# Kernel optimization log

Measured on AMD Instinct MI355X. Metric: run time of the kernel, lower is better.

Reference implementation:

```python
import jax, jax.numpy as jnp
import numpy as np

B = 2048
D = 256
TEMPERATURE = 0.5
EPS = 1e-8  # torch.nn.CosineSimilarity eps


def _neg_indices(b):
    # Static mask: exclude diagonal and positive pairs (i, B+i), (B+i, i).
    n = 2 * b
    mask = np.ones((n, n), dtype=bool)
    np.fill_diagonal(mask, False)
    idx = np.arange(b)
    mask[idx, b + idx] = False
    mask[b + idx, idx] = False
    rows, cols = np.nonzero(mask)  # row-major order, matches torch sim[mask]
    return rows.reshape(n, n - 2), cols.reshape(n, n - 2)

_NEG_ROWS, _NEG_COLS = _neg_indices(B)


def setup_inputs() -> dict:
    key = jax.random.key(0)
    k1, k2 = jax.random.split(key)
    z_i = jax.random.normal(k1, (B, D), dtype=jnp.float32)
    z_j = jax.random.normal(k2, (B, D), dtype=jnp.float32)
    return {"z_i": z_i, "z_j": z_j}


def reference(z_i, z_j):
    b = z_i.shape[0]
    n = 2 * b
    z = jnp.concatenate([z_i, z_j], axis=0)  # [N, D]
    # Cosine similarity = normalize -> matmul (same math as broadcast CosineSimilarity)
    norm = jnp.maximum(jnp.linalg.norm(z, axis=1, keepdims=True), EPS)
    zn = z / norm
    sim = (zn @ zn.T) / TEMPERATURE  # [N, N]
    # positives: diag(sim, B) and diag(sim, -B)
    pos = jnp.concatenate([jnp.diagonal(sim, offset=b), jnp.diagonal(sim, offset=-b)], axis=0)  # [N]
    # negatives: static masked gather -> [N, N-2]
    neg = sim[_NEG_ROWS, _NEG_COLS]
    logits = jnp.concatenate([pos[:, None], neg], axis=1)  # [N, N-1]
    # CrossEntropyLoss(reduction='sum') with labels all zero, then / N
    loss = -jax.nn.log_softmax(logits, axis=1)[:, 0]
    return jnp.sum(loss) / n
```

## Files before the change

### kernel.cpp

```cpp
#include <hip/hip_runtime.h>
#include <hip/hip_bf16.h>
#include <math.h>

#define B_PAIRS 2048
#define N_ROWS  4096
#define D_DIM   256
#define INV_T   2.0f

typedef __attribute__((ext_vector_type(8))) short  short8;
typedef __attribute__((ext_vector_type(4))) float  floatx4;


__device__ __forceinline__ void async_copy16(const void* gsrc, void* ldst) {
    __builtin_amdgcn_global_load_lds(
        (__attribute__((address_space(1))) void*)gsrc,
        (__attribute__((address_space(3))) void*)ldst,
        16, 0, 0);
}

__global__ __launch_bounds__(256)
void ntx_normalize(const float* __restrict__ z_i,
                   const float* __restrict__ z_j,
                   __hip_bfloat16* __restrict__ zn,
                   float* __restrict__ S) {
    const int w    = threadIdx.x >> 6;
    const int lane = threadIdx.x & 63;
    const int row  = blockIdx.x * 4 + w;
    const float* src = (row < B_PAIRS) ? (z_i + (size_t)row * D_DIM)
                                       : (z_j + (size_t)(row - B_PAIRS) * D_DIM);
    const float4 v = *(const float4*)(src + lane * 4);
    float ss = v.x * v.x + v.y * v.y + v.z * v.z + v.w * v.w;
    #pragma unroll
    for (int off = 32; off > 0; off >>= 1) ss += __shfl_xor(ss, off, 64);
    const float rn = 1.0f / fmaxf(sqrtf(ss), 1e-8f);
    union { short4 s4; __hip_bfloat16 h[4]; } u;
    u.h[0] = __float2bfloat16(v.x * rn);
    u.h[1] = __float2bfloat16(v.y * rn);
    u.h[2] = __float2bfloat16(v.z * rn);
    u.h[3] = __float2bfloat16(v.w * rn);
    *(short4*)(void*)(zn + (size_t)row * D_DIM + lane * 4) = u.s4;
    if (lane == 0) S[row] = 0.0f;
}

#define BM 128
#define BN 128
#define BK 32
#define N_TILES 528

__global__ __launch_bounds__(256)
void ntx_simtile(const __hip_bfloat16* __restrict__ zn,
                 float* __restrict__ S,
                 float* __restrict__ pos) {
    __shared__ __align__(16) __hip_bfloat16 As[BM * BK];
    __shared__ __align__(16) __hip_bfloat16 Bs[BN * BK];

    int t = blockIdx.x, by = 0, rowlen = 32;
    while (t >= rowlen) { t -= rowlen; by++; rowlen--; }
    const int bx = by + t;

    const int tid  = threadIdx.x;
    const int lane = tid & 63;
    const int w    = tid >> 6;
    const int wr   = w >> 1;
    const int wc   = w & 1;
    const int quad = lane >> 4;
    const int l16  = lane & 15;

    const int rowA0 = by * BM;
    const int rowB0 = bx * BN;
    const bool isDiag = (rowA0 == rowB0);
    const bool isPos  = (rowB0 == (rowA0 ^ B_PAIRS));

    floatx4 acc[4][4];
    #pragma unroll
    for (int i = 0; i < 4; i++)
        #pragma unroll
        for (int j = 0; j < 4; j++)
            acc[i][j] = (floatx4){0.f, 0.f, 0.f, 0.f};

    for (int k0 = 0; k0 < D_DIM; k0 += BK) {
        #pragma unroll
        for (int c = 0; c < 2; c++) {
            const int chunk = tid + c * 256;
            const int r  = chunk >> 2;
            const int kc = chunk & 3;
            async_copy16(zn + ((size_t)(rowA0 + r) * D_DIM + k0 + kc * 8),
                         As + chunk * 8);
            async_copy16(zn + ((size_t)(rowB0 + r) * D_DIM + k0 + kc * 8),
                         Bs + chunk * 8);
        }
        __syncthreads();

        short8 afr[4], bfr[4];
        #pragma unroll
        for (int fi = 0; fi < 4; fi++) {
            const int ar = wr * 64 + fi * 16 + l16;
            afr[fi] = *(const short8*)(const void*)(As + ar * BK + quad * 8);
        }
        #pragma unroll
        for (int fj = 0; fj < 4; fj++) {
            const int brw = wc * 64 + fj * 16 + l16;
            bfr[fj] = *(const short8*)(const void*)(Bs + brw * BK + quad * 8);
        }
        #pragma unroll
        for (int fi = 0; fi < 4; fi++)
            #pragma unroll
            for (int fj = 0; fj < 4; fj++)
                acc[fi][fj] = __builtin_amdgcn_mfma_f32_16x16x32_bf16(
                    afr[fi], bfr[fj], acc[fi][fj], 0, 0, 0);
        __syncthreads();
    }

    float cs[4] = {0.f, 0.f, 0.f, 0.f};
    #pragma unroll
    for (int fi = 0; fi < 4; fi++) {
        float rs[4] = {0.f, 0.f, 0.f, 0.f};
        #pragma unroll
        for (int fj = 0; fj < 4; fj++) {
            const int rj = wc * 64 + fj * 16 + l16;
            #pragma unroll
            for (int reg = 0; reg < 4; reg++) {
                const int ri = wr * 64 + fi * 16 + quad * 4 + reg;
                const float v = acc[fi][fj][reg] * INV_T;
                const bool d = (ri == rj);
                if (isPos && d) {
                    pos[rowA0 + ri] = v;
                    pos[rowB0 + rj] = v;
                }
                const float e = (isDiag && d) ? 0.f : __expf(v);
                rs[reg] += e;
                cs[fj]  += e;
            }
        }
        #pragma unroll
        for (int reg = 0; reg < 4; reg++) {
            float r = rs[reg];
            r += __shfl_xor(r, 1, 16);
            r += __shfl_xor(r, 2, 16);
            r += __shfl_xor(r, 4, 16);
            r += __shfl_xor(r, 8, 16);
            if (l16 == 0)
                atomicAdd(&S[rowA0 + wr * 64 + fi * 16 + quad * 4 + reg], r);
        }
    }
    if (!isDiag) {
        #pragma unroll
        for (int fj = 0; fj < 4; fj++) {
            float c = cs[fj];
            c += __shfl_xor(c, 16, 64);
            c += __shfl_xor(c, 32, 64);
            if (quad == 0)
                atomicAdd(&S[rowB0 + wc * 64 + fj * 16 + l16], c);
        }
    }
}

__global__ __launch_bounds__(1024)
void ntx_finalize(const float* __restrict__ S,
                  const float* __restrict__ pos,
                  float* __restrict__ out) {
    const int tid = threadIdx.x;
    float acc = 0.f;
    #pragma unroll
    for (int c = 0; c < 4; c++) {
        const int i = tid + c * 1024;
        acc += __logf(S[i]) - pos[i];
    }
    #pragma unroll
    for (int off = 32; off > 0; off >>= 1) acc += __shfl_down(acc, off, 64);
    __shared__ float red[16];
    if ((tid & 63) == 0) red[tid >> 6] = acc;
    __syncthreads();
    if (tid == 0) {
        float s = 0.f;
        #pragma unroll
        for (int k = 0; k < 16; k++) s += red[k];
        out[0] = s / (float)N_ROWS;
    }
}

extern "C" void kernel_launch(void* const* d_in, const int* in_sizes, int n_in,
                              void* d_out, int out_size, void* d_ws, size_t ws_size,
                              hipStream_t stream) {
    const float* z_i = (const float*)d_in[0];
    const float* z_j = (const float*)d_in[1];
    float* out = (float*)d_out;

    __hip_bfloat16* zn = (__hip_bfloat16*)d_ws;
    float* S   = (float*)((char*)d_ws + (size_t)N_ROWS * D_DIM * sizeof(__hip_bfloat16));
    float* pos = S + N_ROWS;

    ntx_normalize<<<N_ROWS / 4, 256, 0, stream>>>(z_i, z_j, zn, S);
    ntx_simtile<<<N_TILES, 256, 0, stream>>>(zn, S, pos);
    ntx_finalize<<<1, 1024, 0, stream>>>(S, pos, out);
}
```

Baseline: 81.48 us.

## Fuse finalize into simtile via last-block reduction and swizzle LDS tiles

Removes the separate finalize kernel. The last tile block to finish, found with an atomic counter, now computes the log-sum and the output. Positive logits are summed per block into one atomic scalar instead of being written to a per-row array. LDS tile loads and reads also get an XOR swizzle on the k-chunk index to reduce bank conflicts on the MFMA fragment loads. The cost is extra atomics and threadfences, plus a serial tail in which a single block reduces 4096 rows.

```diff
diff --git a/kernel.cpp b/kernel.cpp
--- a/kernel.cpp
+++ b/kernel.cpp
@@ -22,7 +22,9 @@
 void ntx_normalize(const float* __restrict__ z_i,
                    const float* __restrict__ z_j,
                    __hip_bfloat16* __restrict__ zn,
-                   float* __restrict__ S) {
+                   float* __restrict__ S,
+                   float* __restrict__ posSum,
+                   unsigned* __restrict__ cnt) {
     const int w    = threadIdx.x >> 6;
     const int lane = threadIdx.x & 63;
     const int row  = blockIdx.x * 4 + w;
@@ -40,6 +42,7 @@
     u.h[3] = __float2bfloat16(v.w * rn);
     *(short4*)(void*)(zn + (size_t)row * D_DIM + lane * 4) = u.s4;
     if (lane == 0) S[row] = 0.0f;
+    if (blockIdx.x == 0 && threadIdx.x == 0) { *posSum = 0.0f; *cnt = 0u; }
 }
 
 #define BM 128
@@ -50,7 +53,9 @@
 __global__ __launch_bounds__(256)
 void ntx_simtile(const __hip_bfloat16* __restrict__ zn,
                  float* __restrict__ S,
-                 float* __restrict__ pos) {
+                 float* __restrict__ posSum,
+                 unsigned* __restrict__ cnt,
+                 float* __restrict__ out) {
     __shared__ __align__(16) __hip_bfloat16 As[BM * BK];
     __shared__ __align__(16) __hip_bfloat16 Bs[BN * BK];
 
@@ -84,9 +89,10 @@
             const int chunk = tid + c * 256;
             const int r  = chunk >> 2;
             const int kc = chunk & 3;
-            async_copy16(zn + ((size_t)(rowA0 + r) * D_DIM + k0 + kc * 8),
+            const int g  = kc ^ ((r >> 1) & 3);
+            async_copy16(zn + ((size_t)(rowA0 + r) * D_DIM + k0 + g * 8),
                          As + chunk * 8);
-            async_copy16(zn + ((size_t)(rowB0 + r) * D_DIM + k0 + kc * 8),
+            async_copy16(zn + ((size_t)(rowB0 + r) * D_DIM + k0 + g * 8),
                          Bs + chunk * 8);
         }
         __syncthreads();
@@ -95,12 +101,14 @@
         #pragma unroll
         for (int fi = 0; fi < 4; fi++) {
             const int ar = wr * 64 + fi * 16 + l16;
-            afr[fi] = *(const short8*)(const void*)(As + ar * BK + quad * 8);
+            const int sk = quad ^ ((ar >> 1) & 3);
+            afr[fi] = *(const short8*)(const void*)(As + ar * BK + sk * 8);
         }
         #pragma unroll
         for (int fj = 0; fj < 4; fj++) {
-            const int brw = wc * 64 + fj * 16 + l16;
-            bfr[fj] = *(const short8*)(const void*)(Bs + brw * BK + quad * 8);
+            const int br = wc * 64 + fj * 16 + l16;
+            const int sk = quad ^ ((br >> 1) & 3);
+            bfr[fj] = *(const short8*)(const void*)(Bs + br * BK + sk * 8);
         }
         #pragma unroll
         for (int fi = 0; fi < 4; fi++)
@@ -112,6 +120,7 @@
     }
 
     float cs[4] = {0.f, 0.f, 0.f, 0.f};
+    float psum = 0.f;
     #pragma unroll
     for (int fi = 0; fi < 4; fi++) {
         float rs[4] = {0.f, 0.f, 0.f, 0.f};
@@ -123,10 +132,7 @@
                 const int ri = wr * 64 + fi * 16 + quad * 4 + reg;
                 const float v = acc[fi][fj][reg] * INV_T;
                 const bool d = (ri == rj);
-                if (isPos && d) {
-                    pos[rowA0 + ri] = v;
-                    pos[rowB0 + rj] = v;
-                }
+                if (isPos && d) psum += 2.0f * v;
                 const float e = (isDiag && d) ? 0.f : __expf(v);
                 rs[reg] += e;
                 cs[fj]  += e;
@@ -153,29 +159,43 @@
                 atomicAdd(&S[rowB0 + wc * 64 + fj * 16 + l16], c);
         }
     }
-}
-
-__global__ __launch_bounds__(1024)
-void ntx_finalize(const float* __restrict__ S,
-                  const float* __restrict__ pos,
-                  float* __restrict__ out) {
-    const int tid = threadIdx.x;
-    float acc = 0.f;
-    #pragma unroll
-    for (int c = 0; c < 4; c++) {
-        const int i = tid + c * 1024;
-        acc += __logf(S[i]) - pos[i];
-    }
-    #pragma unroll
-    for (int off = 32; off > 0; off >>= 1) acc += __shfl_down(acc, off, 64);
-    __shared__ float red[16];
-    if ((tid & 63) == 0) red[tid >> 6] = acc;
+    if (isPos) {
+        psum += __shfl_xor(psum, 1, 64);  psum += __shfl_xor(psum, 2, 64);
+        psum += __shfl_xor(psum, 4, 64);  psum += __shfl_xor(psum, 8, 64);
+        psum += __shfl_xor(psum, 16, 64); psum += __shfl_xor(psum, 32, 64);
+        __shared__ float pred[4];
+        if (lane == 0) pred[w] = psum;
+        __syncthreads();
+        if (tid == 0)
+            atomicAdd(posSum, pred[0] + pred[1] + pred[2] + pred[3]);
+    }
+
+    __shared__ bool amLast;
+    __threadfence();
+    if (tid == 0) {
+        unsigned old = atomicAdd(cnt, 1u);
+        amLast = (old == N_TILES - 1);
+    }
     __syncthreads();
-    if (tid == 0) {
-        float s = 0.f;
-        #pragma unroll
-        for (int k = 0; k < 16; k++) s += red[k];
-        out[0] = s / (float)N_ROWS;
+    if (amLast) {
+        __threadfence();
+        float acc2 = 0.f;
+        for (int i = tid; i < N_ROWS; i += 256) {
+            float s = __hip_atomic_load(&S[i], __ATOMIC_RELAXED,
+                                        __HIP_MEMORY_SCOPE_AGENT);
+            acc2 += __logf(s);
+        }
+        #pragma unroll
+        for (int off = 32; off > 0; off >>= 1) acc2 += __shfl_xor(acc2, off, 64);
+        __shared__ float red[4];
+        if (lane == 0) red[w] = acc2;
+        __syncthreads();
+        if (tid == 0) {
+            float logsum = red[0] + red[1] + red[2] + red[3];
+            float ps = __hip_atomic_load(posSum, __ATOMIC_RELAXED,
+                                         __HIP_MEMORY_SCOPE_AGENT);
+            out[0] = (logsum - ps) / (float)N_ROWS;
+        }
     }
 }
 
@@ -187,10 +207,10 @@
     float* out = (float*)d_out;
 
     __hip_bfloat16* zn = (__hip_bfloat16*)d_ws;
-    float* S   = (float*)((char*)d_ws + (size_t)N_ROWS * D_DIM * sizeof(__hip_bfloat16));
-    float* pos = S + N_ROWS;
-
-    ntx_normalize<<<N_ROWS / 4, 256, 0, stream>>>(z_i, z_j, zn, S);
-    ntx_simtile<<<N_TILES, 256, 0, stream>>>(zn, S, pos);
-    ntx_finalize<<<1, 1024, 0, stream>>>(S, pos, out);
-}
+    float* S        = (float*)((char*)d_ws + (size_t)N_ROWS * D_DIM * sizeof(__hip_bfloat16));
+    float* posSum   = S + N_ROWS;
+    unsigned* cnt   = (unsigned*)(posSum + 1);
+
+    ntx_normalize<<<N_ROWS / 4, 256, 0, stream>>>(z_i, z_j, zn, S, posSum, cnt);
+    ntx_simtile<<<N_TILES, 256, 0, stream>>>(zn, S, posSum, cnt, out);
+}
```

After: 110.3 us. 35.4% more time.
